# Kernel tuning notes

Measured on AMD Instinct MI355X. Metric: run time of the kernel, lower is better.

Reference implementation:

```python
import jax, jax.numpy as jnp
import numpy as np

# Module constants (from init_kwargs)
D_MODEL = 128
N_HEADS = 8
D_H = D_MODEL // N_HEADS
SCALE = D_H ** -0.5
D_IN = 8          # number of channels
SEQ_LEN = 128     # per-channel key length (S = D_IN*SEQ_LEN)


def setup_inputs() -> dict:
    key = jax.random.key(0)
    ks = jax.random.split(key, 16)
    B, P, S = 8, 512, 1024
    Q = jax.random.normal(ks[0], (B, P, D_MODEL), jnp.float32)
    K = jax.random.normal(ks[1], (B, S, D_MODEL), jnp.float32)
    V = jax.random.normal(ks[2], (B, S, D_MODEL), jnp.float32)
    prev = jax.random.normal(ks[3], (B, P, N_HEADS, S), jnp.float32)
    # cross-channel mask: attend only to tokens from a *different* channel
    pred_ch = jnp.arange(P) // (P // D_IN)          # (P,)
    seq_ch = jnp.arange(S) // SEQ_LEN               # (S,)
    attn_mask = (pred_ch[:, None] != seq_ch[None, :]).reshape(1, P, 1, S)
    w = lambda k, shp: jax.random.normal(k, shp, jnp.float32) * 0.02
    Wq, bq = w(ks[4], (D_MODEL, D_MODEL)), w(ks[5], (D_MODEL,))
    Wk, bk = w(ks[6], (D_MODEL, D_MODEL)), w(ks[7], (D_MODEL,))
    Wv, bv = w(ks[8], (D_MODEL, D_MODEL)), w(ks[9], (D_MODEL,))
    Wo, bo = w(ks[10], (D_MODEL, D_MODEL)), w(ks[11], (D_MODEL,))
    ch_gate = jax.random.normal(ks[12], (D_IN, D_IN), jnp.float32)
    return dict(Q=Q, K=K, V=V, prev=prev, attn_mask=attn_mask,
                Wq=Wq, bq=bq, Wk=Wk, bk=bk, Wv=Wv, bv=bv, Wo=Wo, bo=bo,
                ch_gate=ch_gate)


def reference(Q, K, V, prev, attn_mask, Wq, bq, Wk, bk, Wv, bv, Wo, bo, ch_gate):
    B, P, _ = Q.shape
    S = K.shape[1]
    H, dh = N_HEADS, D_H
    q = (Q @ Wq.T + bq).reshape(B, P, H, dh)
    k = (K @ Wk.T + bk).reshape(B, S, H, dh)
    v = (V @ Wv.T + bv).reshape(B, S, H, dh)
    raw_scores = jnp.einsum('bphd,bshd->bphs', q, k) * SCALE
    raw_scores = raw_scores + prev                     # residual attention
    # channel gating with STE
    pred_ch = jnp.arange(P) // (P // D_IN)
    seq_ch = jnp.arange(S) // SEQ_LEN
    s = jax.nn.sigmoid(ch_gate)
    hard = (s >= 0.5).astype(s.dtype)
    gate_ch = hard + (s - jax.lax.stop_gradient(s))
    gate_full = gate_ch[pred_ch][:, seq_ch].reshape(1, P, 1, S)
    raw_scores = jnp.where(jnp.isfinite(raw_scores), raw_scores * gate_full, raw_scores)
    # stable masked softmax with explicit renormalization
    stable = raw_scores - jnp.max(raw_scores, axis=-1, keepdims=True)
    masked = jnp.where(attn_mask, stable, -1e9)
    attn = jax.nn.softmax(masked, axis=-1)
    attn = attn * attn_mask.astype(attn.dtype)
    den = jnp.clip(jnp.sum(attn, axis=-1, keepdims=True), 1e-9, None)
    attn = attn / den
    out = jnp.einsum('bphs,bshd->bphd', attn, v).reshape(B, P, H * dh)
    out = out @ Wo.T + bo
    return out, attn, raw_scores
```

## Files before the change

kernel.cpp:

```cpp
#include <hip/hip_runtime.h>
#include <hip/hip_bf16.h>

typedef unsigned short u16;
typedef float f32x4 __attribute__((ext_vector_type(4)));
typedef __bf16 bf16x8 __attribute__((ext_vector_type(8)));
typedef _Float16 f16x8 __attribute__((ext_vector_type(8)));
typedef _Float16 f16x2 __attribute__((ext_vector_type(2)));

union Frag { int4 i; bf16x8 b; f16x8 h; };

__device__ inline u16 f2bf(float f) {
  union { float f; unsigned u; } v; v.f = f;
  unsigned r = v.u + 0x7FFFu + ((v.u >> 16) & 1u);
  return (u16)(r >> 16);
}
__device__ inline unsigned pk_f16(float a, float b) {
  return __builtin_bit_cast(unsigned, __builtin_amdgcn_cvt_pkrtz(a, b));
}

__device__ __forceinline__
void proj_body(u16* __restrict__ smem,
               const float* __restrict__ X, const float* __restrict__ W,
               const float* __restrict__ bias, void* __restrict__ out,
               int mode, int innerShift, int rows0)
{
  u16* XL = smem;
  u16* WL = smem + 64 * 136;

  const int tid = threadIdx.x;
  const int w = tid >> 6, l = tid & 63, lg = l >> 4, lr = l & 15;

  #pragma unroll
  for (int i = 0; i < 8; ++i) {
    int u = tid + i * 256;
    int rr = u >> 5, c4 = (u & 31) * 4;
    const float4 xv = *(const float4*)(X + (rows0 + rr) * 128 + c4);
    uint2 p;
    p.x = (unsigned)f2bf(xv.x) | ((unsigned)f2bf(xv.y) << 16);
    p.y = (unsigned)f2bf(xv.z) | ((unsigned)f2bf(xv.w) << 16);
    *(uint2*)(XL + rr * 136 + c4) = p;
  }
  #pragma unroll
  for (int i = 0; i < 16; ++i) {
    int u = tid + i * 256;
    int rr = u >> 5, c4 = (u & 31) * 4;
    const float4 xv = *(const float4*)(W + rr * 128 + c4);
    uint2 p;
    p.x = (unsigned)f2bf(xv.x) | ((unsigned)f2bf(xv.y) << 16);
    p.y = (unsigned)f2bf(xv.z) | ((unsigned)f2bf(xv.w) << 16);
    *(uint2*)(WL + rr * 136 + c4) = p;
  }
  __syncthreads();

  Frag a[4];
  #pragma unroll
  for (int kc = 0; kc < 4; ++kc)
    a[kc].i = *(const int4*)(XL + (16 * w + lr) * 136 + kc * 32 + 8 * lg);

  f32x4 acc[8];
  #pragma unroll
  for (int ct = 0; ct < 8; ++ct) {
    f32x4 c = {0.f, 0.f, 0.f, 0.f};
    #pragma unroll
    for (int kc = 0; kc < 4; ++kc) {
      Frag bw;
      bw.i = *(const int4*)(WL + (ct * 16 + lr) * 136 + kc * 32 + 8 * lg);
      c = __builtin_amdgcn_mfma_f32_16x16x32_bf16(a[kc].b, bw.b, c, 0, 0, 0);
    }
    acc[ct] = c;
  }

  if (mode == 2) {
    float* o = (float*)out;
    #pragma unroll
    for (int ct = 0; ct < 8; ++ct) {
      float bn = bias[ct * 16 + lr];
      #pragma unroll
      for (int j = 0; j < 4; ++j) {
        int row = rows0 + 16 * w + 4 * lg + j;
        o[row * 128 + ct * 16 + lr] = acc[ct][j] + bn;
      }
    }
  } else if (mode == 0) {
    u16* o = (u16*)out;
    const int innerMask = (1 << innerShift) - 1;
    #pragma unroll
    for (int ct = 0; ct < 8; ++ct) {
      float bn = bias[ct * 16 + lr];
      #pragma unroll
      for (int j = 0; j < 4; ++j) {
        int row = rows0 + 16 * w + 4 * lg + j;
        int bI = row >> innerShift, r = row & innerMask;
        o[(((bI * 8 + ct) << innerShift) + r) * 16 + lr] =
            __builtin_bit_cast(u16, (_Float16)(acc[ct][j] + bn));
      }
    }
  } else {
    __syncthreads();
    u16* YT = smem;
    #pragma unroll
    for (int ct = 0; ct < 8; ++ct) {
      float bn = bias[ct * 16 + lr];
      #pragma unroll
      for (int j = 0; j < 4; ++j)
        YT[(ct * 16 + lr) * 72 + 16 * w + 4 * lg + j] =
            __builtin_bit_cast(u16, (_Float16)(acc[ct][j] + bn));
    }
    __syncthreads();
    u16* o = (u16*)out;
    const int bI = rows0 >> 10, s0 = rows0 & 1023;
    #pragma unroll
    for (int i = 0; i < 4; ++i) {
      int u = tid + i * 256;
      int n = u >> 3, ch = (u & 7) * 8;
      int4 v = *(const int4*)(YT + n * 72 + ch);
      *(int4*)(o + ((bI * 8 + (n >> 4)) * 16 + (n & 15)) * 1024 + s0 + ch) = v;
    }
  }
}

__global__ __launch_bounds__(256, 2)
void proj_qkv(const float* __restrict__ Q, const float* __restrict__ K,
              const float* __restrict__ V,
              const float* __restrict__ Wq, const float* __restrict__ bq,
              const float* __restrict__ Wk, const float* __restrict__ bk,
              const float* __restrict__ Wv, const float* __restrict__ bv,
              u16* __restrict__ qb, u16* __restrict__ kb, u16* __restrict__ vtb)
{
  __shared__ __attribute__((aligned(16))) u16 smem[26112];
  const int bid = blockIdx.x;
  if (bid < 64)       proj_body(smem, Q, Wq, bq, qb,  0,  9, bid * 64);
  else if (bid < 192) proj_body(smem, K, Wk, bk, kb,  0, 10, (bid - 64) * 64);
  else                proj_body(smem, V, Wv, bv, vtb, 1, 10, (bid - 192) * 64);
}

__global__ __launch_bounds__(256, 2)
void proj_out(const float* __restrict__ X, const float* __restrict__ W,
              const float* __restrict__ bias, float* __restrict__ out)
{
  __shared__ __attribute__((aligned(16))) u16 smem[26112];
  proj_body(smem, X, W, bias, out, 2, 9, blockIdx.x * 64);
}

__global__ __launch_bounds__(256, 4)
void attn_kernel(const u16* __restrict__ qb, const u16* __restrict__ kb,
                 const u16* __restrict__ vtb, const float* __restrict__ prev,
                 const float* __restrict__ ch_gate,
                 float* __restrict__ rs_out, float* __restrict__ attn_out,
                 float* __restrict__ preout)
{
  __shared__ __attribute__((aligned(16))) u16 SRS[16][1032];
  __shared__ float DenInv[16];
  __shared__ float OutBuf[4][16][20];

  const int bid = blockIdx.x;
  const int vb = (bid & 7) * 256 + (bid >> 3);
  const int pt = vb & 31, h = (vb >> 5) & 7, b = vb >> 8;
  const int p0 = pt * 16, ptch = pt >> 2;
  const int tid = threadIdx.x, w = tid >> 6, l = tid & 63;
  const int lg = l >> 4, lr = l & 15;

  unsigned gbits = 0u;
  #pragma unroll
  for (int j = 0; j < 8; ++j)
    if (ch_gate[ptch * 8 + j] >= 0.f) gbits |= (1u << j);
  gbits = __builtin_amdgcn_readfirstlane(gbits);

  const int r = 4 * w + lg;
  const int base = ((b * 512 + p0) * 8 + h) * 1024;
  const float* prow = prev + base + r * 8192;

  const f32x4 zf = {0.f, 0.f, 0.f, 0.f};
  f32x4 pf0 = (gbits & 1u) ? __builtin_nontemporal_load((const f32x4*)(prow +   0 + lr * 4)) : zf;
  f32x4 pf1 = (gbits & 1u) ? __builtin_nontemporal_load((const f32x4*)(prow +  64 + lr * 4)) : zf;
  f32x4 pf2 = (gbits & 2u) ? __builtin_nontemporal_load((const f32x4*)(prow + 128 + lr * 4)) : zf;
  f32x4 pf3 = (gbits & 2u) ? __builtin_nontemporal_load((const f32x4*)(prow + 192 + lr * 4)) : zf;

  Frag aq;
  if (lg < 2) aq.i = *(const int4*)(qb + (((b * 8 + h) * 512 + p0 + lr) * 16 + 8 * lg));
  else        aq.i = make_int4(0, 0, 0, 0);

  const u16* kbase = kb + (b * 8 + h) * 1024 * 16;
  const int sbase = w * 256;

  #pragma unroll 2
  for (int st = 0; st < 16; ++st) {
    const int s0 = sbase + st * 16;
    if (!((gbits >> (s0 >> 7)) & 1u)) continue;
    Frag bk;
    if (lg < 2) bk.i = *(const int4*)(kbase + (s0 + lr) * 16 + 8 * lg);
    else        bk.i = make_int4(0, 0, 0, 0);
    f32x4 zero = {0.f, 0.f, 0.f, 0.f};
    f32x4 d = __builtin_amdgcn_mfma_f32_16x16x32_f16(bk.h, aq.h, zero, 0, 0, 0);
    uint2 pk2;
    pk2.x = pk_f16(d[0] * 0.25f, d[1] * 0.25f);
    pk2.y = pk_f16(d[2] * 0.25f, d[3] * 0.25f);
    *(uint2*)&SRS[lr][s0 + 4 * lg] = pk2;
  }
  __syncthreads();

  float* rsrow = rs_out + base + r * 8192;
  float den = 0.f;
  uint2 eh[16];

  #pragma unroll
  for (int it = 0; it < 16; ++it) {
    const int s = it * 64 + lr * 4;
    const int ch = it >> 1;
    const bool msk = (ch == ptch);
    if ((gbits >> ch) & 1u) {
      f32x4 pv;
      if      (it == 0) pv = pf0;
      else if (it == 1) pv = pf1;
      else if (it == 2) pv = pf2;
      else if (it == 3) pv = pf3;
      else pv = __builtin_nontemporal_load((const f32x4*)(prow + s));
      union { uint2 u; f16x2 hh[2]; } sc;
      sc.u = *(const uint2*)&SRS[r][s];
      f32x4 rs;
      rs[0] = (float)sc.hh[0][0] + pv[0];
      rs[1] = (float)sc.hh[0][1] + pv[1];
      rs[2] = (float)sc.hh[1][0] + pv[2];
      rs[3] = (float)sc.hh[1][1] + pv[3];
      __builtin_nontemporal_store(rs, (f32x4*)(rsrow + s));
      if (msk) {
        eh[it] = make_uint2(0u, 0u);
      } else {
        float e0 = __expf(rs[0]);
        float e1 = __expf(rs[1]);
        float e2 = __expf(rs[2]);
        float e3 = __expf(rs[3]);
        den += (e0 + e1) + (e2 + e3);
        eh[it].x = pk_f16(e0, e1);
        eh[it].y = pk_f16(e2, e3);
      }
    } else {
      __builtin_nontemporal_store(zf, (f32x4*)(rsrow + s));
      if (msk) eh[it] = make_uint2(0u, 0u);
      else   { eh[it] = make_uint2(0x3C003C00u, 0x3C003C00u); den += 4.f; }
    }
    *(uint2*)&SRS[r][s] = eh[it];
  }

  #pragma unroll
  for (int off = 1; off < 16; off <<= 1)
    den += __shfl_xor(den, off);
  const float invd = 1.f / den;
  if (lr == 0) DenInv[r] = invd;

  {
    float* arow = attn_out + base + r * 8192;
    #pragma unroll
    for (int it = 0; it < 16; ++it) {
      const int s = it * 64 + lr * 4;
      union { uint2 u; f16x2 hh[2]; } e;
      e.u = eh[it];
      f32x4 o;
      o[0] = (float)e.hh[0][0] * invd;
      o[1] = (float)e.hh[0][1] * invd;
      o[2] = (float)e.hh[1][0] * invd;
      o[3] = (float)e.hh[1][1] * invd;
      __builtin_nontemporal_store(o, (f32x4*)(arow + s));
    }
  }
  __syncthreads();

  f32x4 acc = {0.f, 0.f, 0.f, 0.f};
  const u16* vbase = vtb + ((b * 8 + h) * 16 + lr) * 1024;
  #pragma unroll
  for (int kc = 0; kc < 8; ++kc) {
    Frag pa, bv;
    pa.i = *(const int4*)(&SRS[lr][sbase + kc * 32 + 8 * lg]);
    bv.i = *(const int4*)(vbase + sbase + kc * 32 + 8 * lg);
    acc = __builtin_amdgcn_mfma_f32_16x16x32_f16(pa.h, bv.h, acc, 0, 0, 0);
  }
  #pragma unroll
  for (int j = 0; j < 4; ++j) OutBuf[w][4 * lg + j][lr] = acc[j];
  __syncthreads();
  {
    const int pr = tid >> 4, dd = tid & 15;
    float o = (OutBuf[0][pr][dd] + OutBuf[1][pr][dd] +
               OutBuf[2][pr][dd] + OutBuf[3][pr][dd]) * DenInv[pr];
    preout[((b * 512 + p0 + pr) * 8 + h) * 16 + dd] = o;
  }
}

extern "C" void kernel_launch(void* const* d_in, const int* in_sizes, int n_in,
                              void* d_out, int out_size, void* d_ws, size_t ws_size,
                              hipStream_t stream)
{
  (void)in_sizes; (void)n_in; (void)out_size; (void)ws_size;
  const float* Q       = (const float*)d_in[0];
  const float* K       = (const float*)d_in[1];
  const float* V       = (const float*)d_in[2];
  const float* prev    = (const float*)d_in[3];
  const float* Wq      = (const float*)d_in[5];
  const float* bq      = (const float*)d_in[6];
  const float* Wk      = (const float*)d_in[7];
  const float* bk      = (const float*)d_in[8];
  const float* Wv      = (const float*)d_in[9];
  const float* bv      = (const float*)d_in[10];
  const float* Wo      = (const float*)d_in[11];
  const float* bo      = (const float*)d_in[12];
  const float* ch_gate = (const float*)d_in[13];

  u16*   qb     = (u16*)d_ws;
  u16*   kb     = qb + 524288;
  u16*   vtb    = kb + 1048576;
  float* preout = (float*)((char*)d_ws + 5242880);

  float* outp     = (float*)d_out;
  float* attn_out = outp + 524288;
  float* rs_out   = outp + 34078720;

  proj_qkv<<<320, 256, 0, stream>>>(Q, K, V, Wq, bq, Wk, bk, Wv, bv,
                                    qb, kb, vtb);
  attn_kernel<<<2048, 256, 0, stream>>>(qb, kb, vtb, prev, ch_gate,
                                        rs_out, attn_out, preout);
  proj_out<<<64, 256, 0, stream>>>(preout, Wo, bo, outp);
}
```

Measured before the change: 108.0 us.

## Swizzle score LDS layout, reuse it for output reduction, raise occupancy

Replaces the padded 16x1032 score buffer with an unpadded XOR-swizzled 16x1024 layout to avoid LDS bank conflicts. The separate DenInv and OutBuf arrays are dropped and their contents are placed into the score buffer after the PV matmul. That cuts LDS per block, and the launch bound rises from 4 to 5 blocks per CU. The PV MFMA and output reduction now run before the normalized attention writes, so that store stream overlaps the tail. This adds an extra barrier and may limit registers per thread under the tighter launch bound.

```diff
diff --git a/kernel.cpp b/kernel.cpp
--- a/kernel.cpp
+++ b/kernel.cpp
@@ -142,16 +142,18 @@
   proj_body(smem, X, W, bias, out, 2, 9, blockIdx.x * 64);
 }
 
-__global__ __launch_bounds__(256, 4)
+__device__ __forceinline__ int swz(int row, int elem) {
+  return row * 1024 + (elem ^ ((row & 7) << 3));
+}
+
+__global__ __launch_bounds__(256, 5)
 void attn_kernel(const u16* __restrict__ qb, const u16* __restrict__ kb,
                  const u16* __restrict__ vtb, const float* __restrict__ prev,
                  const float* __restrict__ ch_gate,
                  float* __restrict__ rs_out, float* __restrict__ attn_out,
                  float* __restrict__ preout)
 {
-  __shared__ __attribute__((aligned(16))) u16 SRS[16][1032];
-  __shared__ float DenInv[16];
-  __shared__ float OutBuf[4][16][20];
+  __shared__ __attribute__((aligned(16))) u16 SRS[16384];
 
   const int bid = blockIdx.x;
   const int vb = (bid & 7) * 256 + (bid >> 3);
@@ -195,7 +197,7 @@
     uint2 pk2;
     pk2.x = pk_f16(d[0] * 0.25f, d[1] * 0.25f);
     pk2.y = pk_f16(d[2] * 0.25f, d[3] * 0.25f);
-    *(uint2*)&SRS[lr][s0 + 4 * lg] = pk2;
+    *(uint2*)&SRS[swz(lr, s0 + 4 * lg)] = pk2;
   }
   __syncthreads();
 
@@ -216,7 +218,7 @@
       else if (it == 3) pv = pf3;
       else pv = __builtin_nontemporal_load((const f32x4*)(prow + s));
       union { uint2 u; f16x2 hh[2]; } sc;
-      sc.u = *(const uint2*)&SRS[r][s];
+      sc.u = *(const uint2*)&SRS[swz(r, s)];
       f32x4 rs;
       rs[0] = (float)sc.hh[0][0] + pv[0];
       rs[1] = (float)sc.hh[0][1] + pv[1];
@@ -239,14 +241,42 @@
       if (msk) eh[it] = make_uint2(0u, 0u);
       else   { eh[it] = make_uint2(0x3C003C00u, 0x3C003C00u); den += 4.f; }
     }
-    *(uint2*)&SRS[r][s] = eh[it];
+    *(uint2*)&SRS[swz(r, s)] = eh[it];
   }
 
   #pragma unroll
   for (int off = 1; off < 16; off <<= 1)
     den += __shfl_xor(den, off);
   const float invd = 1.f / den;
-  if (lr == 0) DenInv[r] = invd;
+  __syncthreads();
+
+  f32x4 acc = {0.f, 0.f, 0.f, 0.f};
+  const u16* vbase = vtb + ((b * 8 + h) * 16 + lr) * 1024;
+  #pragma unroll
+  for (int kc = 0; kc < 8; ++kc) {
+    Frag pa, bv;
+    pa.i = *(const int4*)(&SRS[swz(lr, sbase + kc * 32 + 8 * lg)]);
+    bv.i = *(const int4*)(vbase + sbase + kc * 32 + 8 * lg);
+    acc = __builtin_amdgcn_mfma_f32_16x16x32_f16(pa.h, bv.h, acc, 0, 0, 0);
+  }
+
+  __syncthreads();
+  {
+    float* OutBuf = (float*)SRS;
+    #pragma unroll
+    for (int j = 0; j < 4; ++j)
+      OutBuf[(w * 16 + 4 * lg + j) * 20 + lr] = acc[j];
+    if (lr == 0) OutBuf[1280 + r] = invd;
+  }
+  __syncthreads();
+  {
+    float* OutBuf = (float*)SRS;
+    const int pr = tid >> 4, dd = tid & 15;
+    float o = (OutBuf[pr * 20 + dd] + OutBuf[(16 + pr) * 20 + dd] +
+               OutBuf[(32 + pr) * 20 + dd] + OutBuf[(48 + pr) * 20 + dd]) *
+              OutBuf[1280 + pr];
+    preout[((b * 512 + p0 + pr) * 8 + h) * 16 + dd] = o;
+  }
 
   {
     float* arow = attn_out + base + r * 8192;
@@ -262,26 +292,6 @@
       o[3] = (float)e.hh[1][1] * invd;
       __builtin_nontemporal_store(o, (f32x4*)(arow + s));
     }
-  }
-  __syncthreads();
-
-  f32x4 acc = {0.f, 0.f, 0.f, 0.f};
-  const u16* vbase = vtb + ((b * 8 + h) * 16 + lr) * 1024;
-  #pragma unroll
-  for (int kc = 0; kc < 8; ++kc) {
-    Frag pa, bv;
-    pa.i = *(const int4*)(&SRS[lr][sbase + kc * 32 + 8 * lg]);
-    bv.i = *(const int4*)(vbase + sbase + kc * 32 + 8 * lg);
-    acc = __builtin_amdgcn_mfma_f32_16x16x32_f16(pa.h, bv.h, acc, 0, 0, 0);
-  }
-  #pragma unroll
-  for (int j = 0; j < 4; ++j) OutBuf[w][4 * lg + j][lr] = acc[j];
-  __syncthreads();
-  {
-    const int pr = tid >> 4, dd = tid & 15;
-    float o = (OutBuf[0][pr][dd] + OutBuf[1][pr][dd] +
-               OutBuf[2][pr][dd] + OutBuf[3][pr][dd]) * DenInv[pr];
-    preout[((b * 512 + p0 + pr) * 8 + h) * 16 + dd] = o;
   }
 }
 
```

Measured after the change: 104.8 us. -3.0%, faster.
